# Optimization experiments

Measured on AMD Instinct MI355X. Metric: run time of the kernel, lower is better.

Reference implementation:

```python
import jax, jax.numpy as jnp
import numpy as np

MAX_LEN = 150
DIM_HEAD = 64


def setup_inputs() -> dict:
    key = jax.random.key(0)
    kq, kk, kv, kp, km = jax.random.split(key, 5)
    B, H, L, Dh = 4, 16, 1024, DIM_HEAD
    q = jax.random.normal(kq, (B, H, L, Dh), dtype=jnp.float32)
    k = jax.random.normal(kk, (B, H, L, Dh), dtype=jnp.float32)
    v = jax.random.normal(kv, (B, H, L, Dh), dtype=jnp.float32)
    pos_embedding = jax.random.normal(kp, (2 * MAX_LEN + 1, Dh), dtype=jnp.float32)
    mask = jax.random.randint(km, (B, 1, 1, L), 0, 2).astype(bool)
    return {"q": q, "k": k, "v": v, "pos_embedding": pos_embedding, "mask": mask}


def reference(q, k, v, pos_embedding, mask):
    B, H, Lq, Dh = q.shape
    Lk = k.shape[2]
    scale = jnp.asarray(np.sqrt(Dh), dtype=q.dtype)
    # relative position index: clamp(j - i, -max_len, max_len) + max_len - 1
    # (faithful to source, incl. the -1 offset; index -1 wraps to last row in both torch and jax)
    rel = jnp.arange(Lk)[None, :] - jnp.arange(Lq)[:, None]
    rel_idx = jnp.clip(rel, -MAX_LEN, MAX_LEN) + MAX_LEN - 1  # [Lq, Lk]
    R = pos_embedding[rel_idx]  # [Lq, Lk, Dh]
    # relative-position score: q_t @ R^T  ->  [B, H, Lq, Lk]
    rp = jnp.einsum('bhqd,qkd->bhqk', q, R)
    scores = (jnp.einsum('bhqd,bhkd->bhqk', q, k) + rp) / scale
    scores = jnp.where(mask, -jnp.inf, scores)
    attn = jax.nn.softmax(scores, axis=-1)
    return jnp.einsum('bhqk,bhkd->bhqd', attn, v)
```

## Files before the change

### kernel.cpp

```cpp
#include <hip/hip_runtime.h>
#include <math.h>


#define LL 1024
#define DH 64
#define MAXL 150

typedef __attribute__((ext_vector_type(8)))  short    short8;
typedef __attribute__((ext_vector_type(4)))  float    f32x4;
typedef __attribute__((ext_vector_type(16))) float    f32x16;
typedef __attribute__((ext_vector_type(4)))  unsigned u32x4;

union U4S8 { u32x4 u; short8 s; };

__device__ __forceinline__ unsigned cvtpk(float lo, float hi) {
  unsigned r;
  asm("v_cvt_pk_bf16_f32 %0, %1, %2" : "=v"(r) : "v"(lo), "v"(hi));
  return r;
}
__device__ __forceinline__ float bf2f(unsigned short s) {
  return __uint_as_float((unsigned)s << 16);
}
__device__ __forceinline__ short8 pack8f(float4 a, float4 b) {
  U4S8 t;
  t.u[0] = cvtpk(a.x, a.y); t.u[1] = cvtpk(a.z, a.w);
  t.u[2] = cvtpk(b.x, b.y); t.u[3] = cvtpk(b.z, b.w);
  return t.s;
}
__device__ __forceinline__ int swz(int row, int cb) {
  return row * 128 + (cb ^ ((row & 7) << 4));
}
__device__ __forceinline__ void st_pair(unsigned char* base, int row, int colb,
                                        float a, float b) {
  unsigned u = cvtpk(a, b);
  *(unsigned short*)(base + swz(row, colb))     = (unsigned short)u;
  *(unsigned short*)(base + swz(row + 1, colb)) = (unsigned short)(u >> 16);
}
#define KOFF(r) ((((r) & 3)) + 8 * ((r) >> 2))

__global__ __launch_bounds__(256, 2)
void rp_attn32(const float* __restrict__ Q, const float* __restrict__ K,
               const float* __restrict__ V, const float* __restrict__ POS,
               const int* __restrict__ MSK, float* __restrict__ OUT) {
  __shared__ __attribute__((aligned(16))) unsigned short qrs[64][306];
  __shared__ __attribute__((aligned(16))) unsigned char  kv[32768];
  __shared__ __attribute__((aligned(16))) float          mskf[1024];

  const int tid = threadIdx.x;
  const int F  = blockIdx.x;
  const int gi = F >> 3;
  const int bh = (F & 7) * 8 + (gi >> 4);
  const int i0 = (gi & 15) * 64;
  const int b  = bh >> 4;

  const int wave = tid >> 6, lane = tid & 63;
  const int lo5 = lane & 31, hi = lane >> 5;
  const int qg = wave & 1, kh = wave >> 1;
  const int qloc = qg * 32 + lo5;
  const int irow = i0 + qloc;

  const int rK = tid >> 2, q4 = tid & 3;
  const int kkV = tid & 63, dwV = wave;

  const size_t bo = (size_t)bh * LL * DH;
  const float* qp = Q + bo;
  const float* kp = K + bo;
  const float* vp = V + bo;
  const int*   mrow = MSK + b * LL;

  unsigned char* ksh = kv + kh * 8192;
  unsigned char* vth = kv + 16384 + kh * 8192;

  short8 qB[4];
#pragma unroll
  for (int c = 0; c < 4; ++c) {
    const float* src = qp + (size_t)irow * DH + c * 16 + hi * 8;
    qB[c] = pack8f(*(const float4*)src, *(const float4*)(src + 4));
  }

#pragma unroll
  for (int t2 = 0; t2 < 4; ++t2) {
    const int ix = tid + t2 * 256;
    mskf[ix] = mrow[ix] ? -INFINITY : 0.0f;
  }

  for (int tb = kh; tb < 10; tb += 2) {
    int trow = tb * 32 + lo5; if (trow > 300) trow = 300;
    const float* pr = POS + (size_t)trow * DH;
    f32x16 z;
#pragma unroll
    for (int x = 0; x < 16; ++x) z[x] = 0.f;
#pragma unroll
    for (int c = 0; c < 4; ++c) {
      const float* s2 = pr + c * 16 + hi * 8;
      short8 af = pack8f(*(const float4*)s2, *(const float4*)(s2 + 4));
      z = __builtin_amdgcn_mfma_f32_32x32x16_bf16(af, qB[c], z, 0, 0, 0);
    }
#pragma unroll
    for (int rp = 0; rp < 8; ++rp) {
      const int r = rp * 2;
      int tp = KOFF(r) + 4 * hi + 32 * tb;
      if (tp < 306)
        *(unsigned*)(&qrs[qloc][tp]) = cvtpk(z[r], z[r + 1]);
    }
  }

  const float SC = 0.18033688011112042f;
  float m2 = -1e30f, lsum = 0.f;
  f32x16 acc0, acc1;
#pragma unroll
  for (int x = 0; x < 16; ++x) { acc0[x] = 0.f; acc1[x] = 0.f; }

  float4 kreg[2][4], vreg[2][4];
  auto LOADT = [&](int rdx) {
#pragma unroll
    for (int h = 0; h < 2; ++h) {
      const float* ksrc = kp + (size_t)(h * 512 + rdx * 64 + rK) * DH + q4 * 16;
#pragma unroll
      for (int i = 0; i < 4; ++i) kreg[h][i] = ((const float4*)ksrc)[i];
      const float* vsrc = vp + (size_t)(h * 512 + rdx * 64 + kkV) * DH + dwV * 16;
#pragma unroll
      for (int i = 0; i < 4; ++i) vreg[h][i] = ((const float4*)vsrc)[i];
    }
  };
  LOADT(0);

  for (int rd = 0; rd < 8; ++rd) {
    __syncthreads();
#pragma unroll
    for (int h = 0; h < 2; ++h) {
      unsigned char* kb_ = kv + h * 8192;
      *(short8*)(kb_ + swz(rK, q4 * 32))      = pack8f(kreg[h][0], kreg[h][1]);
      *(short8*)(kb_ + swz(rK, q4 * 32 + 16)) = pack8f(kreg[h][2], kreg[h][3]);
      unsigned char* vb_ = kv + 16384 + h * 8192;
      const int db = dwV * 16, cb2 = kkV * 2;
      st_pair(vb_, db + 0,  cb2, vreg[h][0].x, vreg[h][0].y);
      st_pair(vb_, db + 2,  cb2, vreg[h][0].z, vreg[h][0].w);
      st_pair(vb_, db + 4,  cb2, vreg[h][1].x, vreg[h][1].y);
      st_pair(vb_, db + 6,  cb2, vreg[h][1].z, vreg[h][1].w);
      st_pair(vb_, db + 8,  cb2, vreg[h][2].x, vreg[h][2].y);
      st_pair(vb_, db + 10, cb2, vreg[h][2].z, vreg[h][2].w);
      st_pair(vb_, db + 12, cb2, vreg[h][3].x, vreg[h][3].y);
      st_pair(vb_, db + 14, cb2, vreg[h][3].z, vreg[h][3].w);
    }
    __syncthreads();
    if (rd < 7) LOADT(rd + 1);

    const int j0 = kh * 512 + rd * 64;

    f32x16 st[2];
#pragma unroll
    for (int kb = 0; kb < 2; ++kb) {
      f32x16 z;
#pragma unroll
      for (int x = 0; x < 16; ++x) z[x] = 0.f;
#pragma unroll
      for (int c = 0; c < 4; ++c) {
        short8 kf = *(const short8*)(ksh + swz(kb * 32 + lo5, c * 32 + hi * 16));
        z = __builtin_amdgcn_mfma_f32_32x32x16_bf16(kf, qB[c], z, 0, 0, 0);
      }
      st[kb] = z;
    }

#pragma unroll
    for (int kb = 0; kb < 2; ++kb) {
      const int jb = j0 + kb * 32;
      f32x4 mg[4];
#pragma unroll
      for (int g4 = 0; g4 < 4; ++g4)
        mg[g4] = *(const f32x4*)&mskf[jb + g4 * 8 + 4 * hi];
      const int relmin = jb - (i0 + qg * 32 + 31);
      const int relmax = jb + 31 - (i0 + qg * 32);
      if (relmin >= MAXL) {
        const float bias = bf2f(qrs[qloc][299]);
#pragma unroll
        for (int r = 0; r < 16; ++r)
          st[kb][r] = (st[kb][r] + bias) * SC + mg[r >> 2][r & 3];
      } else if (relmax <= -MAXL) {
        const float bias = bf2f(qrs[qloc][300]);
#pragma unroll
        for (int r = 0; r < 16; ++r)
          st[kb][r] = (st[kb][r] + bias) * SC + mg[r >> 2][r & 3];
      } else {
#pragma unroll
        for (int r = 0; r < 16; ++r) {
          const int rel = jb + KOFF(r) + 4 * hi - irow;
          const int idx = rel <= -MAXL ? 300 : (rel >= MAXL ? 299 : rel + MAXL - 1);
          st[kb][r] = (st[kb][r] + bf2f(qrs[qloc][idx])) * SC + mg[r >> 2][r & 3];
        }
      }
    }

    f32x16 mx;
#pragma unroll
    for (int r = 0; r < 16; ++r) mx[r] = fmaxf(st[0][r], st[1][r]);
#pragma unroll
    for (int w = 8; w > 0; w >>= 1)
#pragma unroll
      for (int r = 0; r < 8; ++r)
        if (r < w) mx[r] = fmaxf(mx[r], mx[r + w]);
    const float tmax = fmaxf(mx[0], __shfl_xor(mx[0], 32));
    if (!__all(tmax - m2 <= 12.0f)) {
      const float mnew = fmaxf(m2, tmax);
      const float alpha = exp2f(m2 - mnew);
      lsum *= alpha;
      acc0 *= alpha; acc1 *= alpha;
      m2 = mnew;
    }
#pragma unroll
    for (int kb = 0; kb < 2; ++kb)
#pragma unroll
      for (int r = 0; r < 16; ++r) st[kb][r] = exp2f(st[kb][r] - m2);
    f32x16 sx;
#pragma unroll
    for (int r = 0; r < 16; ++r) sx[r] = st[0][r] + st[1][r];
#pragma unroll
    for (int w = 8; w > 0; w >>= 1)
#pragma unroll
      for (int r = 0; r < 8; ++r)
        if (r < w) sx[r] = sx[r] + sx[r + w];
    lsum += sx[0] + __shfl_xor(sx[0], 32);

    short8 pf[4];
#pragma unroll
    for (int ch = 0; ch < 4; ++ch) {
      const int kb = ch >> 1, rb2 = (ch & 1) * 8;
      unsigned a  = cvtpk(st[kb][rb2 + 0], st[kb][rb2 + 1]);
      unsigned a2 = cvtpk(st[kb][rb2 + 2], st[kb][rb2 + 3]);
      unsigned bb = cvtpk(st[kb][rb2 + 4], st[kb][rb2 + 5]);
      unsigned b2 = cvtpk(st[kb][rb2 + 6], st[kb][rb2 + 7]);
      unsigned sa  = __shfl_xor(a, 32);
      unsigned sa2 = __shfl_xor(a2, 32);
      unsigned sbb = __shfl_xor(bb, 32);
      unsigned sb2 = __shfl_xor(b2, 32);
      U4S8 t;
      t.u[0] = hi ? sbb : a;
      t.u[1] = hi ? sb2 : a2;
      t.u[2] = hi ? bb  : sa;
      t.u[3] = hi ? b2  : sa2;
      pf[ch] = t.s;
    }

#pragma unroll
    for (int ch = 0; ch < 4; ++ch) {
      short8 vf0 = *(const short8*)(vth + swz(lo5,      ch * 32 + hi * 16));
      short8 vf1 = *(const short8*)(vth + swz(32 + lo5, ch * 32 + hi * 16));
      acc0 = __builtin_amdgcn_mfma_f32_32x32x16_bf16(vf0, pf[ch], acc0, 0, 0, 0);
      acc1 = __builtin_amdgcn_mfma_f32_32x32x16_bf16(vf1, pf[ch], acc1, 0, 0, 0);
    }
  }

  __syncthreads();
  float* mb = (float*)kv;
  if (wave >= 2) {
    float* d = mb + ((wave - 2) * 64 + lane) * 37;
    d[0] = m2; d[1] = lsum;
#pragma unroll
    for (int r = 0; r < 16; ++r) { d[2 + r] = acc0[r]; d[18 + r] = acc1[r]; }
  }
  __syncthreads();
  if (wave < 2) {
    const float* d = mb + (wave * 64 + lane) * 37;
    const float m1 = d[0], l1 = d[1];
    const float mf = fmaxf(m2, m1);
    const float a0 = exp2f(m2 - mf), a1 = exp2f(m1 - mf);
    const float lf = lsum * a0 + l1 * a1;
    const float inv = 1.f / lf;
    float* op = OUT + bo + (size_t)irow * DH;
#pragma unroll
    for (int r = 0; r < 16; ++r) {
      const int d0 = KOFF(r) + 4 * hi;
      op[d0]      = (acc0[r] * a0 + d[2 + r]  * a1) * inv;
      op[d0 + 32] = (acc1[r] * a0 + d[18 + r] * a1) * inv;
    }
  }
}

extern "C" void kernel_launch(void* const* d_in, const int* in_sizes, int n_in,
                              void* d_out, int out_size, void* d_ws, size_t ws_size,
                              hipStream_t stream) {
  const float* q   = (const float*)d_in[0];
  const float* k   = (const float*)d_in[1];
  const float* v   = (const float*)d_in[2];
  const float* pos = (const float*)d_in[3];
  const int*   msk = (const int*)d_in[4];
  float* out = (float*)d_out;

  rp_attn32<<<dim3(1024), dim3(256), 0, stream>>>(q, k, v, pos, msk, out);
}
```

Baseline: 95.13 us.

## Load K/V fragments directly from global memory instead of staging through LDS

Removes the shared-memory staging buffers and the register prefetch pipeline for K and V. Each wave now reads its K and V MFMA operands straight from global memory, converts them to bf16 in registers, and no longer synchronises inside the main loop. The smaller LDS footprint lets launch bounds ask for three blocks per CU instead of two. In exchange, the two q-group waves that share a key half each fetch the same K/V data, which doubles global/L2 traffic. Load latency is also no longer hidden by the earlier one-step prefetch.

```diff
diff --git a/kernel.cpp b/kernel.cpp
--- a/kernel.cpp
+++ b/kernel.cpp
@@ -27,24 +27,19 @@
   t.u[2] = cvtpk(b.x, b.y); t.u[3] = cvtpk(b.z, b.w);
   return t.s;
 }
-__device__ __forceinline__ int swz(int row, int cb) {
-  return row * 128 + (cb ^ ((row & 7) << 4));
-}
-__device__ __forceinline__ void st_pair(unsigned char* base, int row, int colb,
-                                        float a, float b) {
-  unsigned u = cvtpk(a, b);
-  *(unsigned short*)(base + swz(row, colb))     = (unsigned short)u;
-  *(unsigned short*)(base + swz(row + 1, colb)) = (unsigned short)(u >> 16);
-}
 #define KOFF(r) ((((r) & 3)) + 8 * ((r) >> 2))
 
-__global__ __launch_bounds__(256, 2)
+#define QRS_STRIDE 306
+#define OFF_MSK 39168
+#define SMEM_SZ 43264
+
+__global__ __launch_bounds__(256, 3)
 void rp_attn32(const float* __restrict__ Q, const float* __restrict__ K,
                const float* __restrict__ V, const float* __restrict__ POS,
                const int* __restrict__ MSK, float* __restrict__ OUT) {
-  __shared__ __attribute__((aligned(16))) unsigned short qrs[64][306];
-  __shared__ __attribute__((aligned(16))) unsigned char  kv[32768];
-  __shared__ __attribute__((aligned(16))) float          mskf[1024];
+  __shared__ __attribute__((aligned(16))) unsigned char smem[SMEM_SZ];
+  unsigned short* qrs16 = (unsigned short*)smem;
+  float*          mskf  = (float*)(smem + OFF_MSK);
 
   const int tid = threadIdx.x;
   const int F  = blockIdx.x;
@@ -59,18 +54,12 @@
   const int qloc = qg * 32 + lo5;
   const int irow = i0 + qloc;
 
-  const int rK = tid >> 2, q4 = tid & 3;
-  const int kkV = tid & 63, dwV = wave;
-
   const size_t bo = (size_t)bh * LL * DH;
   const float* qp = Q + bo;
   const float* kp = K + bo;
   const float* vp = V + bo;
   const int*   mrow = MSK + b * LL;
 
-  unsigned char* ksh = kv + kh * 8192;
-  unsigned char* vth = kv + 16384 + kh * 8192;
-
   short8 qB[4];
 #pragma unroll
   for (int c = 0; c < 4; ++c) {
@@ -101,9 +90,10 @@
       const int r = rp * 2;
       int tp = KOFF(r) + 4 * hi + 32 * tb;
       if (tp < 306)
-        *(unsigned*)(&qrs[qloc][tp]) = cvtpk(z[r], z[r + 1]);
-    }
-  }
+        *(unsigned*)(&qrs16[qloc * QRS_STRIDE + tp]) = cvtpk(z[r], z[r + 1]);
+    }
+  }
+  __syncthreads();
 
   const float SC = 0.18033688011112042f;
   float m2 = -1e30f, lsum = 0.f;
@@ -111,42 +101,18 @@
 #pragma unroll
   for (int x = 0; x < 16; ++x) { acc0[x] = 0.f; acc1[x] = 0.f; }
 
-  float4 kreg[2][4], vreg[2][4];
-  auto LOADT = [&](int rdx) {
-#pragma unroll
-    for (int h = 0; h < 2; ++h) {
-      const float* ksrc = kp + (size_t)(h * 512 + rdx * 64 + rK) * DH + q4 * 16;
-#pragma unroll
-      for (int i = 0; i < 4; ++i) kreg[h][i] = ((const float4*)ksrc)[i];
-      const float* vsrc = vp + (size_t)(h * 512 + rdx * 64 + kkV) * DH + dwV * 16;
-#pragma unroll
-      for (int i = 0; i < 4; ++i) vreg[h][i] = ((const float4*)vsrc)[i];
-    }
-  };
-  LOADT(0);
-
   for (int rd = 0; rd < 8; ++rd) {
-    __syncthreads();
-#pragma unroll
-    for (int h = 0; h < 2; ++h) {
-      unsigned char* kb_ = kv + h * 8192;
-      *(short8*)(kb_ + swz(rK, q4 * 32))      = pack8f(kreg[h][0], kreg[h][1]);
-      *(short8*)(kb_ + swz(rK, q4 * 32 + 16)) = pack8f(kreg[h][2], kreg[h][3]);
-      unsigned char* vb_ = kv + 16384 + h * 8192;
-      const int db = dwV * 16, cb2 = kkV * 2;
-      st_pair(vb_, db + 0,  cb2, vreg[h][0].x, vreg[h][0].y);
-      st_pair(vb_, db + 2,  cb2, vreg[h][0].z, vreg[h][0].w);
-      st_pair(vb_, db + 4,  cb2, vreg[h][1].x, vreg[h][1].y);
-      st_pair(vb_, db + 6,  cb2, vreg[h][1].z, vreg[h][1].w);
-      st_pair(vb_, db + 8,  cb2, vreg[h][2].x, vreg[h][2].y);
-      st_pair(vb_, db + 10, cb2, vreg[h][2].z, vreg[h][2].w);
-      st_pair(vb_, db + 12, cb2, vreg[h][3].x, vreg[h][3].y);
-      st_pair(vb_, db + 14, cb2, vreg[h][3].z, vreg[h][3].w);
-    }
-    __syncthreads();
-    if (rd < 7) LOADT(rd + 1);
-
     const int j0 = kh * 512 + rd * 64;
+
+    short8 kf[2][4];
+#pragma unroll
+    for (int kb = 0; kb < 2; ++kb) {
+      const float* krp = kp + (size_t)(j0 + kb * 32 + lo5) * DH + hi * 8;
+#pragma unroll
+      for (int c = 0; c < 4; ++c)
+        kf[kb][c] = pack8f(*(const float4*)(krp + c * 16),
+                           *(const float4*)(krp + c * 16 + 4));
+    }
 
     f32x16 st[2];
 #pragma unroll
@@ -155,10 +121,8 @@
 #pragma unroll
       for (int x = 0; x < 16; ++x) z[x] = 0.f;
 #pragma unroll
-      for (int c = 0; c < 4; ++c) {
-        short8 kf = *(const short8*)(ksh + swz(kb * 32 + lo5, c * 32 + hi * 16));
-        z = __builtin_amdgcn_mfma_f32_32x32x16_bf16(kf, qB[c], z, 0, 0, 0);
-      }
+      for (int c = 0; c < 4; ++c)
+        z = __builtin_amdgcn_mfma_f32_32x32x16_bf16(kf[kb][c], qB[c], z, 0, 0, 0);
       st[kb] = z;
     }
 
@@ -169,15 +133,16 @@
 #pragma unroll
       for (int g4 = 0; g4 < 4; ++g4)
         mg[g4] = *(const f32x4*)&mskf[jb + g4 * 8 + 4 * hi];
+      const unsigned short* qrow = &qrs16[qloc * QRS_STRIDE];
       const int relmin = jb - (i0 + qg * 32 + 31);
       const int relmax = jb + 31 - (i0 + qg * 32);
       if (relmin >= MAXL) {
-        const float bias = bf2f(qrs[qloc][299]);
+        const float bias = bf2f(qrow[299]);
 #pragma unroll
         for (int r = 0; r < 16; ++r)
           st[kb][r] = (st[kb][r] + bias) * SC + mg[r >> 2][r & 3];
       } else if (relmax <= -MAXL) {
-        const float bias = bf2f(qrs[qloc][300]);
+        const float bias = bf2f(qrow[300]);
 #pragma unroll
         for (int r = 0; r < 16; ++r)
           st[kb][r] = (st[kb][r] + bias) * SC + mg[r >> 2][r & 3];
@@ -186,7 +151,7 @@
         for (int r = 0; r < 16; ++r) {
           const int rel = jb + KOFF(r) + 4 * hi - irow;
           const int idx = rel <= -MAXL ? 300 : (rel >= MAXL ? 299 : rel + MAXL - 1);
-          st[kb][r] = (st[kb][r] + bf2f(qrs[qloc][idx])) * SC + mg[r >> 2][r & 3];
+          st[kb][r] = (st[kb][r] + bf2f(qrow[idx])) * SC + mg[r >> 2][r & 3];
         }
       }
     }
@@ -243,15 +208,22 @@
 
 #pragma unroll
     for (int ch = 0; ch < 4; ++ch) {
-      short8 vf0 = *(const short8*)(vth + swz(lo5,      ch * 32 + hi * 16));
-      short8 vf1 = *(const short8*)(vth + swz(32 + lo5, ch * 32 + hi * 16));
-      acc0 = __builtin_amdgcn_mfma_f32_32x32x16_bf16(vf0, pf[ch], acc0, 0, 0, 0);
-      acc1 = __builtin_amdgcn_mfma_f32_32x32x16_bf16(vf1, pf[ch], acc1, 0, 0, 0);
+      const float* vcp = vp + (size_t)(j0 + ch * 16 + hi * 8) * DH + lo5;
+      U4S8 w0, w1;
+#pragma unroll
+      for (int p2 = 0; p2 < 4; ++p2) {
+        const float x0 = vcp[(2 * p2) * DH],      x1 = vcp[(2 * p2 + 1) * DH];
+        const float y0 = vcp[(2 * p2) * DH + 32], y1 = vcp[(2 * p2 + 1) * DH + 32];
+        w0.u[p2] = cvtpk(x0, x1);
+        w1.u[p2] = cvtpk(y0, y1);
+      }
+      acc0 = __builtin_amdgcn_mfma_f32_32x32x16_bf16(w0.s, pf[ch], acc0, 0, 0, 0);
+      acc1 = __builtin_amdgcn_mfma_f32_32x32x16_bf16(w1.s, pf[ch], acc1, 0, 0, 0);
     }
   }
 
   __syncthreads();
-  float* mb = (float*)kv;
+  float* mb = (float*)smem;
   if (wave >= 2) {
     float* d = mb + ((wave - 2) * 64 + lane) * 37;
     d[0] = m2; d[1] = lsum;
```

New measurement: 204.2 us. 2.15x slower.
